# Kernel optimization log

Hardware: AMD Instinct MI355X
Metric: run time of the kernel (lower is better)

Reference implementation:

```python
import jax, jax.numpy as jnp
import numpy as np

B, NA, NB = 2, 2048, 2048
DIM_A, DIM_B = 256, 256
HEADS, DH_A, DH_B = 8, 64, 64
INNER_A, INNER_B = DH_A * HEADS, DH_B * HEADS
EPS = 1e-5


def layer_norm(x, w, b):
    m = jnp.mean(x, axis=-1, keepdims=True)
    v = jnp.mean(jnp.square(x - m), axis=-1, keepdims=True)
    return (x - m) * jax.lax.rsqrt(v + EPS) * w + b


def setup_inputs() -> dict:
    key = jax.random.key(0)
    ks = jax.random.split(key, 16)
    s = 0.02
    return {
        "feat_a": jax.random.normal(ks[0], (B, NA, DIM_A), jnp.float32),
        "feat_b": jax.random.normal(ks[1], (B, NB, DIM_B), jnp.float32),
        "mask_a_b": jax.random.bernoulli(ks[2], 0.5, (B, NA, NB)),
        # linear weights stored (in, out)
        "Wq": jax.random.normal(ks[3], (DIM_A, INNER_B), jnp.float32) * s,
        "bq": jnp.zeros((INNER_B,), jnp.float32),
        "Wk": jax.random.normal(ks[4], (DIM_B, INNER_B), jnp.float32) * s,
        "bk": jnp.zeros((INNER_B,), jnp.float32),
        "Wv": jax.random.normal(ks[5], (DIM_B, INNER_A), jnp.float32) * s,
        "bv": jnp.zeros((INNER_A,), jnp.float32),
        "Wg": jax.random.normal(ks[6], (DIM_A, INNER_A), jnp.float32) * s,
        "bg": jnp.zeros((INNER_A,), jnp.float32),
        "Wo": jax.random.normal(ks[7], (INNER_A, DIM_A), jnp.float32) * s,
        "bo": jnp.zeros((DIM_A,), jnp.float32),
        "ln_a_w": jnp.ones((DIM_A,), jnp.float32),
        "ln_a_b": jnp.zeros((DIM_A,), jnp.float32),
        "ln_b_w": jnp.ones((DIM_B,), jnp.float32),
        "ln_b_b": jnp.zeros((DIM_B,), jnp.float32),
        "qln_w": jnp.ones((INNER_B,), jnp.float32),
        "qln_b": jnp.zeros((INNER_B,), jnp.float32),
        "kln_w": jnp.ones((INNER_B,), jnp.float32),
        "kln_b": jnp.zeros((INNER_B,), jnp.float32),
    }


def reference(feat_a, feat_b, mask_a_b, Wq, bq, Wk, bk, Wv, bv, Wg, bg, Wo, bo,
              ln_a_w, ln_a_b, ln_b_w, ln_b_b, qln_w, qln_b, kln_w, kln_b):
    scale = DH_B ** -0.5
    fa = layer_norm(feat_a, ln_a_w, ln_a_b)            # (b, na, dim_a)
    fb = layer_norm(feat_b, ln_b_w, ln_b_b)            # (b, nb, dim_b)
    q = layer_norm(fa @ Wq + bq, qln_w, qln_b)         # (b, na, inner_b)
    k = layer_norm(fb @ Wk + bk, kln_w, kln_b)         # (b, nb, inner_b)
    v = fb @ Wv + bv                                   # (b, nb, inner_a)
    g = fa @ Wg + bg                                   # (b, na, inner_a)
    q = q.reshape(B, NA, HEADS, DH_B)
    k = k.reshape(B, NB, HEADS, DH_B)
    v = v.reshape(B, NB, HEADS, DH_A)
    g = g.reshape(B, NA, HEADS, DH_A)
    sim = jnp.einsum('bihd,bjhd->bhij', q, k) * scale  # (b, h, na, nb)
    neg = jnp.finfo(sim.dtype).min
    sim = jnp.where(mask_a_b[:, None, :, :], sim, neg)
    attn = jax.nn.softmax(sim, axis=-1)
    out = jnp.einsum('bhij,bjhd->bihd', attn, v)       # (b, na, h, dh_a)
    out = jax.nn.sigmoid(g) * out
    out = out.reshape(B, NA, INNER_A)
    return out @ Wo + bo                               # (b, na, dim_a)
```

## Files before the change

kernel.cpp:

```cpp
#include <hip/hip_runtime.h>
#include <hip/hip_bf16.h>

using bf16 = __hip_bfloat16;
typedef short bf16x8 __attribute__((ext_vector_type(8)));
typedef short bf16x4 __attribute__((ext_vector_type(4)));
typedef float f32x4 __attribute__((ext_vector_type(4)));
typedef unsigned short ushort8_t __attribute__((ext_vector_type(8)));
typedef unsigned long long u64;

static constexpr int NA_ = 2048, NB_ = 2048;
static constexpr int H_ = 8, DH_ = 64, INNER_ = 512;
static constexpr int MROWS = 2 * NA_;

#define MFMA32(a, b, c) __builtin_amdgcn_mfma_f32_16x16x32_bf16(a, b, c, 0, 0, 0)

#if __has_builtin(__builtin_amdgcn_mfma_f32_16x16x16bf16_1k)
#define HAS_MFMA16 1
#define MFMA16(a, b, c) __builtin_amdgcn_mfma_f32_16x16x16bf16_1k(a, b, c, 0, 0, 0)
#elif __has_builtin(__builtin_amdgcn_mfma_f32_16x16x16_bf16)
#define HAS_MFMA16 1
#define MFMA16(a, b, c) __builtin_amdgcn_mfma_f32_16x16x16_bf16(a, b, c, 0, 0, 0)
#else
#define HAS_MFMA16 0
#endif

__device__ __forceinline__ unsigned short bfbits(float x) {
  bf16 h = __float2bfloat16(x);
  return __builtin_bit_cast(unsigned short, h);
}
__device__ __forceinline__ float b2f(unsigned short u) {
  unsigned v = ((unsigned)u) << 16;
  return __builtin_bit_cast(float, v);
}

__global__ __launch_bounds__(256) void ln_feat_kernel(
    const float* __restrict__ fa_in, const float* __restrict__ fb_in,
    const float* __restrict__ law, const float* __restrict__ lab,
    const float* __restrict__ lbw, const float* __restrict__ lbb,
    bf16* __restrict__ fa, bf16* __restrict__ fb) {
  int row = blockIdx.x * 4 + (threadIdx.x >> 6);
  int lane = threadIdx.x & 63;
  const float *src, *w, *bb;
  bf16* dst;
  int r;
  if (row < MROWS) { src = fa_in; w = law; bb = lab; dst = fa; r = row; }
  else             { src = fb_in; w = lbw; bb = lbb; dst = fb; r = row - MROWS; }
  float4 x = *(const float4*)(src + (size_t)r * 256 + lane * 4);
  float s  = (x.x + x.y) + (x.z + x.w);
  float s2 = (x.x * x.x + x.y * x.y) + (x.z * x.z + x.w * x.w);
#pragma unroll
  for (int m = 32; m >= 1; m >>= 1) { s += __shfl_xor(s, m); s2 += __shfl_xor(s2, m); }
  float mean = s * (1.0f / 256.0f);
  float var  = s2 * (1.0f / 256.0f) - mean * mean;
  float rstd = rsqrtf(var + 1e-5f);
  float4 wv = *(const float4*)(w + lane * 4);
  float4 bv = *(const float4*)(bb + lane * 4);
  ushort4 o;
  o.x = bfbits((x.x - mean) * rstd * wv.x + bv.x);
  o.y = bfbits((x.y - mean) * rstd * wv.y + bv.y);
  o.z = bfbits((x.z - mean) * rstd * wv.z + bv.z);
  o.w = bfbits((x.w - mean) * rstd * wv.w + bv.w);
  *(ushort4*)(dst + (size_t)r * 256 + lane * 4) = o;
}

__global__ __launch_bounds__(256) void wconv_kernel(
    const float* __restrict__ Wq, const float* __restrict__ Wk,
    const float* __restrict__ Wv, const float* __restrict__ Wg,
    const float* __restrict__ Wo,
    bf16* __restrict__ Wqt, bf16* __restrict__ Wkt,
    bf16* __restrict__ Wvt, bf16* __restrict__ Wgt,
    bf16* __restrict__ Woth, bf16* __restrict__ Wotl) {
  int z = blockIdx.z;
  int idx = blockIdx.x * 256 + threadIdx.x;
  if (z < 4) {
    const float* W = (z == 0) ? Wq : (z == 1) ? Wk : (z == 2) ? Wv : Wg;
    bf16* Wt = (z == 0) ? Wqt : (z == 1) ? Wkt : (z == 2) ? Wvt : Wgt;
    int kk = idx >> 9, n = idx & 511;
    Wt[n * 256 + kk] = __float2bfloat16(W[idx]);
  } else {
    int kk = idx >> 8, n = idx & 255;
    float w = Wo[idx];
    bf16 hi = __float2bfloat16(w);
    Woth[n * 512 + kk] = hi;
    Wotl[n * 512 + kk] = __float2bfloat16(w - __bfloat162float(hi));
  }
}

__global__ void maskdetect_kernel(const unsigned char* __restrict__ m, int* __restrict__ flag) {
  int t = threadIdx.x;
  if (t == 0) *flag = 0;
  __syncthreads();
  if ((t & 3) != 0 && m[t] != 0) atomicOr(flag, 1);
}

__global__ __launch_bounds__(256) void maskpack_kernel(
    const void* __restrict__ maskp, const int* __restrict__ mflag,
    u64* __restrict__ mbits) {
  const bool m8 = (*mflag != 0);
  int lane = threadIdx.x & 63;
  int wid = threadIdx.x >> 6;
  const size_t NW = 131072;
  for (size_t word = (size_t)blockIdx.x * 4 + wid; word < NW; word += (size_t)gridDim.x * 4) {
    size_t e = word * 64 + lane;
    int v = m8 ? (int)((const unsigned char*)maskp)[e] : ((const int*)maskp)[e];
    u64 bal = __ballot(v != 0);
    if (lane == 0) mbits[word] = bal;
  }
}

__global__ __launch_bounds__(512) void qk_ln_gemm_kernel(
    const bf16* __restrict__ fa, const bf16* __restrict__ fb,
    const bf16* __restrict__ Wqt, const bf16* __restrict__ Wkt,
    const float* __restrict__ bq, const float* __restrict__ bk,
    const float* __restrict__ qlw, const float* __restrict__ qlb,
    const float* __restrict__ klw, const float* __restrict__ klb,
    bf16* __restrict__ qo, bf16* __restrict__ ko) {
  __shared__ __align__(16) bf16 As[32 * 264];
  __shared__ float Pred[32 * 16];
  __shared__ float MV[64];
  int z = blockIdx.y;
  const bf16* A    = z ? fb : fa;
  const bf16* Wt   = z ? Wkt : Wqt;
  const float* bias = z ? bk : bq;
  const float* lw  = z ? klw : qlw;
  const float* lb  = z ? klb : qlb;
  bf16* out        = z ? ko : qo;
  int m0 = blockIdx.x * 32;
  int t = threadIdx.x, wave = t >> 6, lane = t & 63;
  int lm = lane & 15, quad = lane >> 4, q8 = quad * 8;
  int n0w = wave * 64;
#pragma unroll
  for (int i = 0; i < 2; i++) {
    int id = t + 512 * i, r = id >> 5, cg = id & 31;
    *(ushort8_t*)(&As[r * 264 + cg * 8]) =
        *(const ushort8_t*)(A + (size_t)(m0 + r) * 256 + cg * 8);
  }
  __syncthreads();
  f32x4 acc[2][4] = {};
  const bf16* wrow[4];
#pragma unroll
  for (int ni = 0; ni < 4; ni++) wrow[ni] = Wt + (size_t)(n0w + ni * 16 + lm) * 256;
#pragma unroll
  for (int ks = 0; ks < 8; ks++) {
    int k0 = ks * 32;
    bf16x8 bf_[4], af[2];
#pragma unroll
    for (int ni = 0; ni < 4; ni++) bf_[ni] = *(const bf16x8*)(wrow[ni] + k0 + q8);
#pragma unroll
    for (int mi = 0; mi < 2; mi++)
      af[mi] = *(const bf16x8*)(&As[(mi * 16 + lm) * 264 + k0 + q8]);
#pragma unroll
    for (int mi = 0; mi < 2; mi++)
#pragma unroll
      for (int ni = 0; ni < 4; ni++)
        acc[mi][ni] = MFMA32(af[mi], bf_[ni], acc[mi][ni]);
  }
  float bv[4];
#pragma unroll
  for (int ni = 0; ni < 4; ni++) bv[ni] = bias[n0w + ni * 16 + lm];
#pragma unroll
  for (int mi = 0; mi < 2; mi++)
#pragma unroll
    for (int ni = 0; ni < 4; ni++)
#pragma unroll
      for (int r = 0; r < 4; r++) acc[mi][ni][r] += bv[ni];
#pragma unroll
  for (int mi = 0; mi < 2; mi++)
#pragma unroll
    for (int r = 0; r < 4; r++) {
      float s  = (acc[mi][0][r] + acc[mi][1][r]) + (acc[mi][2][r] + acc[mi][3][r]);
      float s2 = (acc[mi][0][r] * acc[mi][0][r] + acc[mi][1][r] * acc[mi][1][r]) +
                 (acc[mi][2][r] * acc[mi][2][r] + acc[mi][3][r] * acc[mi][3][r]);
#pragma unroll
      for (int m = 1; m <= 8; m <<= 1) { s += __shfl_xor(s, m); s2 += __shfl_xor(s2, m); }
      if (lm == 0) {
        int row = mi * 16 + quad * 4 + r;
        Pred[row * 16 + wave * 2]     = s;
        Pred[row * 16 + wave * 2 + 1] = s2;
      }
    }
  __syncthreads();
  if (t < 32) {
    float s = 0.f, s2 = 0.f;
#pragma unroll
    for (int w = 0; w < 8; w++) { s += Pred[t * 16 + w * 2]; s2 += Pred[t * 16 + w * 2 + 1]; }
    float mean = s * (1.0f / 512.0f);
    float var  = s2 * (1.0f / 512.0f) - mean * mean;
    MV[t * 2]     = mean;
    MV[t * 2 + 1] = rsqrtf(var + 1e-5f);
  }
  __syncthreads();
  float lww[4], lbb_[4];
#pragma unroll
  for (int ni = 0; ni < 4; ni++) { lww[ni] = lw[n0w + ni * 16 + lm]; lbb_[ni] = lb[n0w + ni * 16 + lm]; }
#pragma unroll
  for (int mi = 0; mi < 2; mi++)
#pragma unroll
    for (int r = 0; r < 4; r++) {
      int row = mi * 16 + quad * 4 + r;
      float mean = MV[row * 2], rstd = MV[row * 2 + 1];
      size_t obase = (size_t)(m0 + row) * 512 + n0w;
#pragma unroll
      for (int ni = 0; ni < 4; ni++)
        out[obase + ni * 16 + lm] =
            __float2bfloat16((acc[mi][ni][r] - mean) * rstd * lww[ni] + lbb_[ni]);
    }
}

__global__ __launch_bounds__(256) void gv_gemm_kernel(
    const bf16* __restrict__ fa, const bf16* __restrict__ fb,
    const bf16* __restrict__ Wgt, const bf16* __restrict__ Wvt,
    const float* __restrict__ bg, const float* __restrict__ bv,
    bf16* __restrict__ gout, bf16* __restrict__ vout) {
  constexpr int K = 256;
  __shared__ __align__(16) bf16 As[64 * 72];
  __shared__ __align__(16) bf16 Bs[64 * 72];
  int z = blockIdx.z;
  const bf16* A    = z ? fb : fa;
  const bf16* Wt   = z ? Wvt : Wgt;
  const float* bias = z ? bv : bg;
  int n0 = blockIdx.x * 64, m0 = blockIdx.y * 64;
  int t = threadIdx.x, wave = t >> 6, lane = t & 63;
  int lm = lane & 15, quad = lane >> 4, q8 = quad * 8;
  int wm = (wave & 1) * 32, wn = (wave >> 1) * 32;
  f32x4 acc[2][2] = {};
  for (int k0 = 0; k0 < K; k0 += 64) {
    __syncthreads();
#pragma unroll
    for (int i = 0; i < 2; i++) {
      int id = t + 256 * i, r = id >> 3, cg = id & 7;
      *(ushort8_t*)(&As[r * 72 + cg * 8]) =
          *(const ushort8_t*)(A + (size_t)(m0 + r) * K + k0 + cg * 8);
      *(ushort8_t*)(&Bs[r * 72 + cg * 8]) =
          *(const ushort8_t*)(Wt + (size_t)(n0 + r) * K + k0 + cg * 8);
    }
    __syncthreads();
#pragma unroll
    for (int kk = 0; kk < 64; kk += 32) {
      bf16x8 af[2], bf_[2];
#pragma unroll
      for (int i = 0; i < 2; i++) {
        af[i]  = *(const bf16x8*)(&As[(wm + i * 16 + lm) * 72 + kk + q8]);
        bf_[i] = *(const bf16x8*)(&Bs[(wn + i * 16 + lm) * 72 + kk + q8]);
      }
#pragma unroll
      for (int mi = 0; mi < 2; mi++)
#pragma unroll
        for (int ni = 0; ni < 2; ni++)
          acc[mi][ni] = MFMA32(af[mi], bf_[ni], acc[mi][ni]);
    }
  }
  if (z == 0) {
#pragma unroll
    for (int mi = 0; mi < 2; mi++)
#pragma unroll
      for (int ni = 0; ni < 2; ni++) {
        int nn = n0 + wn + ni * 16 + lm;
        float bvv = bias[nn];
        int mb = m0 + wm + mi * 16 + quad * 4;
#pragma unroll
        for (int r = 0; r < 4; r++)
          gout[(size_t)(mb + r) * 512 + nn] = __float2bfloat16(acc[mi][ni][r] + bvv);
      }
  } else {
    __syncthreads();
#pragma unroll
    for (int mi = 0; mi < 2; mi++)
#pragma unroll
      for (int ni = 0; ni < 2; ni++) {
        int d_local = wn + ni * 16 + lm;
        float bvv = bias[n0 + d_local];
        int j_local = wm + mi * 16 + quad * 4;
#pragma unroll
        for (int r = 0; r < 4; r++)
          As[d_local * 72 + j_local + r] = __float2bfloat16(acc[mi][ni][r] + bvv);
      }
    __syncthreads();
    int bidx = m0 >> 11, j0g = m0 & 2047;
    int hh = n0 >> 6;
    int dl = t >> 2, jc = (t & 3) * 16;
    bf16* dstrow = vout + (size_t)((bidx * 8 + hh) * 64 + dl) * 2048 + j0g + jc;
#pragma unroll
    for (int c = 0; c < 4; c++)
      *(ushort4*)(dstrow + c * 4) = *(const ushort4*)(&As[dl * 72 + jc + c * 4]);
  }
}

__global__ __launch_bounds__(256) void attn_kernel(
    const bf16* __restrict__ q, const bf16* __restrict__ k,
    const bf16* __restrict__ vt, const bf16* __restrict__ g,
    const u64* __restrict__ mbits,
    bf16* __restrict__ gh, bf16* __restrict__ gl) {
  __shared__ __align__(16) char smem[45056];
  bf16* Qs = (bf16*)smem;
  bf16* Ks = (bf16*)(smem + 9216);
  bf16* Vs = (bf16*)(smem + 27648);
#if !HAS_MFMA16
  __shared__ __align__(16) bf16 Ps[4][16 * 136];
#endif
  int qt = blockIdx.x, bh = blockIdx.y;
  int bidx = bh >> 3, h = bh & 7;
  int i0 = qt * 64;
  int t = threadIdx.x, wave = t >> 6, lane = t & 63;
  int lm = lane & 15, quad = lane >> 4, q8 = quad * 8;

#pragma unroll
  for (int i = 0; i < 2; i++) {
    int id = t + 256 * i, r = id >> 3, cg = id & 7;
    *(ushort8_t*)(&Qs[r * 72 + cg * 8]) =
        *(const ushort8_t*)(q + (size_t)(bidx * NA_ + i0 + r) * INNER_ + h * DH_ + cg * 8);
  }
  __syncthreads();
  bf16x8 bq0 = *(const bf16x8*)(&Qs[(wave * 16 + lm) * 72 + q8]);
  bf16x8 bq1 = *(const bf16x8*)(&Qs[(wave * 16 + lm) * 72 + 32 + q8]);

  f32x4 oT[4] = {};
  float psum = 0.f;
  const float scale2 = 0.125f * 1.44269504088896f;

  const bf16* kb = k + (size_t)(bidx * NB_) * INNER_ + h * DH_;
  const bf16* vb = vt + (size_t)(bh * DH_) * NB_;
  const u64* mrp = mbits + (size_t)(bidx * NA_ + i0 + wave * 16 + lm) * (NB_ / 64);

  for (int it = 0; it < 16; it++) {
    int j0 = it * 128;
    __syncthreads();
#pragma unroll
    for (int i = 0; i < 4; i++) {
      int id = t + 256 * i;
      {
        int r = id >> 3, cg = id & 7;
        *(ushort8_t*)(&Ks[r * 72 + cg * 8]) =
            *(const ushort8_t*)(kb + (size_t)(j0 + r) * INNER_ + cg * 8);
      }
      {
        int d = id >> 4, jg = id & 15;
        *(ushort8_t*)(&Vs[d * 136 + jg * 8]) =
            *(const ushort8_t*)(vb + (size_t)d * NB_ + j0 + jg * 8);
      }
    }
    u64 w0 = mrp[it * 2] >> (quad * 4);
    u64 w1 = mrp[it * 2 + 1] >> (quad * 4);
    __syncthreads();

    f32x4 st[8];
#pragma unroll
    for (int nt = 0; nt < 8; nt++) {
      bf16x8 a0 = *(const bf16x8*)(&Ks[(nt * 16 + lm) * 72 + q8]);
      bf16x8 a1 = *(const bf16x8*)(&Ks[(nt * 16 + lm) * 72 + 32 + q8]);
      f32x4 a = {0.f, 0.f, 0.f, 0.f};
      a = MFMA32(a0, bq0, a);
      a = MFMA32(a1, bq1, a);
      st[nt] = a;
    }

    bf16x4 pf[8];
#pragma unroll
    for (int nt = 0; nt < 8; nt++) {
      u64 wsel = (nt < 4) ? w0 : w1;
      int base = (nt & 3) * 16;
#pragma unroll
      for (int r = 0; r < 4; r++) {
        float p = exp2f(st[nt][r] * scale2 - 16.0f);
        unsigned live = (unsigned)(wsel >> (base + r)) & 1u;
        st[nt][r] = live ? p : 0.0f;
      }
      psum += (st[nt][0] + st[nt][1]) + (st[nt][2] + st[nt][3]);
      bf16x4 pk;
      pk[0] = (short)bfbits(st[nt][0]);
      pk[1] = (short)bfbits(st[nt][1]);
      pk[2] = (short)bfbits(st[nt][2]);
      pk[3] = (short)bfbits(st[nt][3]);
      pf[nt] = pk;
    }

#if HAS_MFMA16
#pragma unroll
    for (int nt = 0; nt < 8; nt++) {
#pragma unroll
      for (int c = 0; c < 4; c++) {
        bf16x4 vf = *(const bf16x4*)(&Vs[(c * 16 + lm) * 136 + nt * 16 + quad * 4]);
        oT[c] = MFMA16(vf, pf[nt], oT[c]);
      }
    }
#else
#pragma unroll
    for (int nt = 0; nt < 8; nt++)
      *(bf16x4*)(&Ps[wave][lm * 136 + nt * 16 + quad * 4]) = pf[nt];
#pragma unroll
    for (int kb4 = 0; kb4 < 4; kb4++) {
      bf16x8 pfr = *(const bf16x8*)(&Ps[wave][lm * 136 + kb4 * 32 + q8]);
#pragma unroll
      for (int c = 0; c < 4; c++) {
        bf16x8 vf = *(const bf16x8*)(&Vs[(c * 16 + lm) * 136 + kb4 * 32 + q8]);
        oT[c] = MFMA32(vf, pfr, oT[c]);
      }
    }
#endif
  }

  psum += __shfl_xor(psum, 16);
  psum += __shfl_xor(psum, 32);
  float inv = 1.0f / psum;

  size_t gbase = (size_t)(bidx * NA_ + i0 + wave * 16 + lm) * INNER_ + h * DH_;
#pragma unroll
  for (int c = 0; c < 4; c++) {
    int dbase = c * 16 + quad * 4;
    bf16x4 gv4 = *(const bf16x4*)(g + gbase + dbase);
    bf16x4 oh, ol;
#pragma unroll
    for (int r = 0; r < 4; r++) {
      float gvf = b2f((unsigned short)gv4[r]);
      float sig = 1.0f / (1.0f + __expf(-gvf));
      float val = oT[c][r] * inv * sig;
      unsigned short hb = bfbits(val);
      oh[r] = (short)hb;
      ol[r] = (short)bfbits(val - b2f(hb));
    }
    *(bf16x4*)(gh + gbase + dbase) = oh;
    *(bf16x4*)(gl + gbase + dbase) = ol;
  }
}

__global__ __launch_bounds__(256) void gemm_split_kernel(
    const bf16* __restrict__ Ah, const bf16* __restrict__ Al,
    const bf16* __restrict__ Bh, const bf16* __restrict__ Bl,
    const float* __restrict__ bias, float* __restrict__ C) {
  constexpr int K = 512, N = 256;
  __shared__ __align__(16) bf16 Ash[32 * 72];
  __shared__ __align__(16) bf16 Asl[32 * 72];
  __shared__ __align__(16) bf16 Bsh[64 * 72];
  __shared__ __align__(16) bf16 Bsl[64 * 72];
  int n0 = blockIdx.x * 64, m0 = blockIdx.y * 32;
  int t = threadIdx.x, wave = t >> 6, lane = t & 63;
  int lm = lane & 15, quad = lane >> 4, q8 = quad * 8;
  int wm = (wave & 1) * 16, wn = (wave >> 1) * 32;
  f32x4 acc[2] = {};
  for (int k0 = 0; k0 < K; k0 += 64) {
    __syncthreads();
    {
      int r = t >> 3, cg = t & 7;
      size_t ga = (size_t)(m0 + r) * K + k0 + cg * 8;
      *(ushort8_t*)(&Ash[r * 72 + cg * 8]) = *(const ushort8_t*)(Ah + ga);
      *(ushort8_t*)(&Asl[r * 72 + cg * 8]) = *(const ushort8_t*)(Al + ga);
    }
#pragma unroll
    for (int i = 0; i < 2; i++) {
      int id = t + 256 * i, r = id >> 3, cg = id & 7;
      size_t gb = (size_t)(n0 + r) * K + k0 + cg * 8;
      *(ushort8_t*)(&Bsh[r * 72 + cg * 8]) = *(const ushort8_t*)(Bh + gb);
      *(ushort8_t*)(&Bsl[r * 72 + cg * 8]) = *(const ushort8_t*)(Bl + gb);
    }
    __syncthreads();
#pragma unroll
    for (int kk = 0; kk < 64; kk += 32) {
      bf16x8 ah = *(const bf16x8*)(&Ash[(wm + lm) * 72 + kk + q8]);
      bf16x8 al = *(const bf16x8*)(&Asl[(wm + lm) * 72 + kk + q8]);
#pragma unroll
      for (int ni = 0; ni < 2; ni++) {
        bf16x8 bh_ = *(const bf16x8*)(&Bsh[(wn + ni * 16 + lm) * 72 + kk + q8]);
        bf16x8 bl_ = *(const bf16x8*)(&Bsl[(wn + ni * 16 + lm) * 72 + kk + q8]);
        acc[ni] = MFMA32(ah, bh_, acc[ni]);
        acc[ni] = MFMA32(ah, bl_, acc[ni]);
        acc[ni] = MFMA32(al, bh_, acc[ni]);
      }
    }
  }
#pragma unroll
  for (int ni = 0; ni < 2; ni++) {
    int n = n0 + wn + ni * 16 + lm;
    float bvv = bias[n];
    int mb = m0 + wm + quad * 4;
#pragma unroll
    for (int r = 0; r < 4; r++) C[(size_t)(mb + r) * N + n] = acc[ni][r] + bvv;
  }
}

extern "C" void kernel_launch(void* const* d_in, const int* in_sizes, int n_in,
                              void* d_out, int out_size, void* d_ws, size_t ws_size,
                              hipStream_t stream) {
  const float* feat_a = (const float*)d_in[0];
  const float* feat_b = (const float*)d_in[1];
  const void*  mask   = d_in[2];
  const float* Wq = (const float*)d_in[3];
  const float* bq = (const float*)d_in[4];
  const float* Wk = (const float*)d_in[5];
  const float* bk = (const float*)d_in[6];
  const float* Wv = (const float*)d_in[7];
  const float* bv = (const float*)d_in[8];
  const float* Wg = (const float*)d_in[9];
  const float* bg = (const float*)d_in[10];
  const float* Wo = (const float*)d_in[11];
  const float* bo = (const float*)d_in[12];
  const float* law = (const float*)d_in[13];
  const float* lab = (const float*)d_in[14];
  const float* lbw = (const float*)d_in[15];
  const float* lbb = (const float*)d_in[16];
  const float* qlw = (const float*)d_in[17];
  const float* qlb = (const float*)d_in[18];
  const float* klw = (const float*)d_in[19];
  const float* klb = (const float*)d_in[20];

  char* ws = (char*)d_ws;
  size_t off = 0;
  auto alloc = [&](size_t bytes) -> void* {
    void* p = ws + off;
    off += (bytes + 255) & ~(size_t)255;
    return p;
  };
  bf16* fa    = (bf16*)alloc((size_t)MROWS * 256 * 2);
  bf16* fb    = (bf16*)alloc((size_t)MROWS * 256 * 2);
  bf16* Wqt   = (bf16*)alloc((size_t)131072 * 2);
  bf16* Wkt   = (bf16*)alloc((size_t)131072 * 2);
  bf16* Wvt   = (bf16*)alloc((size_t)131072 * 2);
  bf16* Wgt   = (bf16*)alloc((size_t)131072 * 2);
  bf16* Woth  = (bf16*)alloc((size_t)131072 * 2);
  bf16* Wotl  = (bf16*)alloc((size_t)131072 * 2);
  bf16* qb_   = (bf16*)alloc((size_t)MROWS * 512 * 2);
  bf16* kb_   = (bf16*)alloc((size_t)MROWS * 512 * 2);
  bf16* vtb   = (bf16*)alloc((size_t)1024 * 2048 * 2);
  bf16* gbuf  = (bf16*)alloc((size_t)MROWS * 512 * 2);
  bf16* gh    = (bf16*)alloc((size_t)MROWS * 512 * 2);
  bf16* gl    = (bf16*)alloc((size_t)MROWS * 512 * 2);
  u64*  mbits = (u64*)alloc((size_t)131072 * 8);
  int*  mflag = (int*)alloc(256);

  ln_feat_kernel<<<2048, 256, 0, stream>>>(feat_a, feat_b, law, lab, lbw, lbb, fa, fb);
  wconv_kernel<<<dim3(512, 1, 5), 256, 0, stream>>>(Wq, Wk, Wv, Wg, Wo, Wqt, Wkt, Wvt, Wgt, Woth, Wotl);
  maskdetect_kernel<<<1, 256, 0, stream>>>((const unsigned char*)mask, mflag);
  maskpack_kernel<<<2048, 256, 0, stream>>>(mask, mflag, mbits);
  qk_ln_gemm_kernel<<<dim3(128, 2), 512, 0, stream>>>(fa, fb, Wqt, Wkt, bq, bk, qlw, qlb, klw, klb, qb_, kb_);
  gv_gemm_kernel<<<dim3(8, 64, 2), 256, 0, stream>>>(fa, fb, Wgt, Wvt, bg, bv, gbuf, vtb);
  attn_kernel<<<dim3(32, 16), 256, 0, stream>>>(qb_, kb_, vtb, gbuf, mbits, gh, gl);
  gemm_split_kernel<<<dim3(4, 128), 256, 0, stream>>>(gh, gl, Woth, Wotl, bo, (float*)d_out);
}
```

Measured before the change: 234.5 us.

## Merge prep kernels, fuse four projection GEMMs, split attention keys across wave halves

The layernorm, weight conversion, mask detection and mask packing launches are merged into one prep kernel, and the Q/K and G/V projection GEMMs are merged into a single launch with retiled blocks. The attention kernel now runs 512 threads, with two groups of four waves each covering half of the key range. The partial outputs and softmax sums are combined through shared memory, and P goes through LDS into 16x16x32 MFMAs instead of the 16x16x16 path. The aim is fewer launches and more latency hiding in attention, at the cost of extra shared memory, a final reduction step, and scalar stores in the epilogue.

After: 204.0 us. 1.15x faster.

```diff
diff --git a/kernel.cpp b/kernel.cpp
--- a/kernel.cpp
+++ b/kernel.cpp
@@ -3,7 +3,6 @@
 
 using bf16 = __hip_bfloat16;
 typedef short bf16x8 __attribute__((ext_vector_type(8)));
-typedef short bf16x4 __attribute__((ext_vector_type(4)));
 typedef float f32x4 __attribute__((ext_vector_type(4)));
 typedef unsigned short ushort8_t __attribute__((ext_vector_type(8)));
 typedef unsigned long long u64;
@@ -14,16 +13,6 @@
 
 #define MFMA32(a, b, c) __builtin_amdgcn_mfma_f32_16x16x32_bf16(a, b, c, 0, 0, 0)
 
-#if __has_builtin(__builtin_amdgcn_mfma_f32_16x16x16bf16_1k)
-#define HAS_MFMA16 1
-#define MFMA16(a, b, c) __builtin_amdgcn_mfma_f32_16x16x16bf16_1k(a, b, c, 0, 0, 0)
-#elif __has_builtin(__builtin_amdgcn_mfma_f32_16x16x16_bf16)
-#define HAS_MFMA16 1
-#define MFMA16(a, b, c) __builtin_amdgcn_mfma_f32_16x16x16_bf16(a, b, c, 0, 0, 0)
-#else
-#define HAS_MFMA16 0
-#endif
-
 __device__ __forceinline__ unsigned short bfbits(float x) {
   bf16 h = __float2bfloat16(x);
   return __builtin_bit_cast(unsigned short, h);
@@ -33,319 +22,309 @@
   return __builtin_bit_cast(float, v);
 }
 
-__global__ __launch_bounds__(256) void ln_feat_kernel(
+__global__ __launch_bounds__(256) void prep_kernel(
     const float* __restrict__ fa_in, const float* __restrict__ fb_in,
     const float* __restrict__ law, const float* __restrict__ lab,
     const float* __restrict__ lbw, const float* __restrict__ lbb,
-    bf16* __restrict__ fa, bf16* __restrict__ fb) {
-  int row = blockIdx.x * 4 + (threadIdx.x >> 6);
-  int lane = threadIdx.x & 63;
-  const float *src, *w, *bb;
-  bf16* dst;
-  int r;
-  if (row < MROWS) { src = fa_in; w = law; bb = lab; dst = fa; r = row; }
-  else             { src = fb_in; w = lbw; bb = lbb; dst = fb; r = row - MROWS; }
-  float4 x = *(const float4*)(src + (size_t)r * 256 + lane * 4);
-  float s  = (x.x + x.y) + (x.z + x.w);
-  float s2 = (x.x * x.x + x.y * x.y) + (x.z * x.z + x.w * x.w);
-#pragma unroll
-  for (int m = 32; m >= 1; m >>= 1) { s += __shfl_xor(s, m); s2 += __shfl_xor(s2, m); }
-  float mean = s * (1.0f / 256.0f);
-  float var  = s2 * (1.0f / 256.0f) - mean * mean;
-  float rstd = rsqrtf(var + 1e-5f);
-  float4 wv = *(const float4*)(w + lane * 4);
-  float4 bv = *(const float4*)(bb + lane * 4);
-  ushort4 o;
-  o.x = bfbits((x.x - mean) * rstd * wv.x + bv.x);
-  o.y = bfbits((x.y - mean) * rstd * wv.y + bv.y);
-  o.z = bfbits((x.z - mean) * rstd * wv.z + bv.z);
-  o.w = bfbits((x.w - mean) * rstd * wv.w + bv.w);
-  *(ushort4*)(dst + (size_t)r * 256 + lane * 4) = o;
-}
-
-__global__ __launch_bounds__(256) void wconv_kernel(
+    bf16* __restrict__ fa, bf16* __restrict__ fb,
     const float* __restrict__ Wq, const float* __restrict__ Wk,
     const float* __restrict__ Wv, const float* __restrict__ Wg,
     const float* __restrict__ Wo,
     bf16* __restrict__ Wqt, bf16* __restrict__ Wkt,
     bf16* __restrict__ Wvt, bf16* __restrict__ Wgt,
-    bf16* __restrict__ Woth, bf16* __restrict__ Wotl) {
-  int z = blockIdx.z;
-  int idx = blockIdx.x * 256 + threadIdx.x;
-  if (z < 4) {
-    const float* W = (z == 0) ? Wq : (z == 1) ? Wk : (z == 2) ? Wv : Wg;
-    bf16* Wt = (z == 0) ? Wqt : (z == 1) ? Wkt : (z == 2) ? Wvt : Wgt;
-    int kk = idx >> 9, n = idx & 511;
-    Wt[n * 256 + kk] = __float2bfloat16(W[idx]);
+    bf16* __restrict__ Woth, bf16* __restrict__ Wotl,
+    const void* __restrict__ maskp, u64* __restrict__ mbits) {
+  int blk = blockIdx.x;
+  int t = threadIdx.x;
+  if (blk < 2048) {
+    int row = blk * 4 + (t >> 6);
+    int lane = t & 63;
+    const float *src, *w, *bb;
+    bf16* dst;
+    int r;
+    if (row < MROWS) { src = fa_in; w = law; bb = lab; dst = fa; r = row; }
+    else             { src = fb_in; w = lbw; bb = lbb; dst = fb; r = row - MROWS; }
+    float4 x = *(const float4*)(src + (size_t)r * 256 + lane * 4);
+    float s  = (x.x + x.y) + (x.z + x.w);
+    float s2 = (x.x * x.x + x.y * x.y) + (x.z * x.z + x.w * x.w);
+#pragma unroll
+    for (int m = 32; m >= 1; m >>= 1) { s += __shfl_xor(s, m); s2 += __shfl_xor(s2, m); }
+    float mean = s * (1.0f / 256.0f);
+    float var  = s2 * (1.0f / 256.0f) - mean * mean;
+    float rstd = rsqrtf(var + 1e-5f);
+    float4 wv = *(const float4*)(w + lane * 4);
+    float4 bv = *(const float4*)(bb + lane * 4);
+    ushort4 o;
+    o.x = bfbits((x.x - mean) * rstd * wv.x + bv.x);
+    o.y = bfbits((x.y - mean) * rstd * wv.y + bv.y);
+    o.z = bfbits((x.z - mean) * rstd * wv.z + bv.z);
+    o.w = bfbits((x.w - mean) * rstd * wv.w + bv.w);
+    *(ushort4*)(dst + (size_t)r * 256 + lane * 4) = o;
+  } else if (blk < 4608) {
+    int z = (blk - 2048) >> 9;
+    int idx = ((blk - 2048) & 511) * 256 + t;
+    if (z < 4) {
+      const float* W = (z == 0) ? Wq : (z == 1) ? Wk : (z == 2) ? Wv : Wg;
+      bf16* Wt = (z == 0) ? Wqt : (z == 1) ? Wkt : (z == 2) ? Wvt : Wgt;
+      int kk = idx >> 9, n = idx & 511;
+      Wt[n * 256 + kk] = __float2bfloat16(W[idx]);
+    } else {
+      int kk = idx >> 8, n = idx & 255;
+      float w = Wo[idx];
+      bf16 hi = __float2bfloat16(w);
+      Woth[n * 512 + kk] = hi;
+      Wotl[n * 512 + kk] = __float2bfloat16(w - __bfloat162float(hi));
+    }
   } else {
-    int kk = idx >> 8, n = idx & 255;
-    float w = Wo[idx];
-    bf16 hi = __float2bfloat16(w);
-    Woth[n * 512 + kk] = hi;
-    Wotl[n * 512 + kk] = __float2bfloat16(w - __bfloat162float(hi));
-  }
-}
-
-__global__ void maskdetect_kernel(const unsigned char* __restrict__ m, int* __restrict__ flag) {
-  int t = threadIdx.x;
-  if (t == 0) *flag = 0;
-  __syncthreads();
-  if ((t & 3) != 0 && m[t] != 0) atomicOr(flag, 1);
-}
-
-__global__ __launch_bounds__(256) void maskpack_kernel(
-    const void* __restrict__ maskp, const int* __restrict__ mflag,
-    u64* __restrict__ mbits) {
-  const bool m8 = (*mflag != 0);
-  int lane = threadIdx.x & 63;
-  int wid = threadIdx.x >> 6;
-  const size_t NW = 131072;
-  for (size_t word = (size_t)blockIdx.x * 4 + wid; word < NW; word += (size_t)gridDim.x * 4) {
-    size_t e = word * 64 + lane;
-    int v = m8 ? (int)((const unsigned char*)maskp)[e] : ((const int*)maskp)[e];
-    u64 bal = __ballot(v != 0);
-    if (lane == 0) mbits[word] = bal;
-  }
-}
-
-__global__ __launch_bounds__(512) void qk_ln_gemm_kernel(
+    __shared__ unsigned shf[4];
+    const unsigned char* mu = (const unsigned char*)maskp;
+    bool nz = ((t & 3) != 0) && (mu[t] != 0);
+    u64 bal = __ballot(nz);
+    if ((t & 63) == 0) shf[t >> 6] = (bal != 0ull) ? 1u : 0u;
+    __syncthreads();
+    bool m8 = (shf[0] | shf[1] | shf[2] | shf[3]) != 0;
+    int lane = t & 63, wid = t >> 6;
+    int lb = blk - 4608;
+    for (size_t word = (size_t)lb * 4 + wid; word < 131072; word += 8192) {
+      size_t e = word * 64 + lane;
+      int v = m8 ? (int)mu[e] : ((const int*)maskp)[e];
+      u64 b2 = __ballot(v != 0);
+      if (lane == 0) mbits[word] = b2;
+    }
+  }
+}
+
+__global__ __launch_bounds__(256) void gemm4_kernel(
     const bf16* __restrict__ fa, const bf16* __restrict__ fb,
     const bf16* __restrict__ Wqt, const bf16* __restrict__ Wkt,
+    const bf16* __restrict__ Wgt, const bf16* __restrict__ Wvt,
     const float* __restrict__ bq, const float* __restrict__ bk,
+    const float* __restrict__ bg, const float* __restrict__ bv,
     const float* __restrict__ qlw, const float* __restrict__ qlb,
     const float* __restrict__ klw, const float* __restrict__ klb,
-    bf16* __restrict__ qo, bf16* __restrict__ ko) {
-  __shared__ __align__(16) bf16 As[32 * 264];
-  __shared__ float Pred[32 * 16];
-  __shared__ float MV[64];
-  int z = blockIdx.y;
-  const bf16* A    = z ? fb : fa;
-  const bf16* Wt   = z ? Wkt : Wqt;
-  const float* bias = z ? bk : bq;
-  const float* lw  = z ? klw : qlw;
-  const float* lb  = z ? klb : qlb;
-  bf16* out        = z ? ko : qo;
-  int m0 = blockIdx.x * 32;
+    bf16* __restrict__ qo, bf16* __restrict__ ko,
+    bf16* __restrict__ gout, bf16* __restrict__ vout) {
+  __shared__ __align__(16) char sm[27648];
+  int z = blockIdx.z;
   int t = threadIdx.x, wave = t >> 6, lane = t & 63;
   int lm = lane & 15, quad = lane >> 4, q8 = quad * 8;
-  int n0w = wave * 64;
-#pragma unroll
-  for (int i = 0; i < 2; i++) {
-    int id = t + 512 * i, r = id >> 5, cg = id & 31;
-    *(ushort8_t*)(&As[r * 264 + cg * 8]) =
-        *(const ushort8_t*)(A + (size_t)(m0 + r) * 256 + cg * 8);
-  }
-  __syncthreads();
-  f32x4 acc[2][4] = {};
-  const bf16* wrow[4];
-#pragma unroll
-  for (int ni = 0; ni < 4; ni++) wrow[ni] = Wt + (size_t)(n0w + ni * 16 + lm) * 256;
-#pragma unroll
-  for (int ks = 0; ks < 8; ks++) {
-    int k0 = ks * 32;
-    bf16x8 bf_[4], af[2];
-#pragma unroll
-    for (int ni = 0; ni < 4; ni++) bf_[ni] = *(const bf16x8*)(wrow[ni] + k0 + q8);
-#pragma unroll
-    for (int mi = 0; mi < 2; mi++)
-      af[mi] = *(const bf16x8*)(&As[(mi * 16 + lm) * 264 + k0 + q8]);
-#pragma unroll
-    for (int mi = 0; mi < 2; mi++)
-#pragma unroll
-      for (int ni = 0; ni < 4; ni++)
-        acc[mi][ni] = MFMA32(af[mi], bf_[ni], acc[mi][ni]);
-  }
-  float bv[4];
-#pragma unroll
-  for (int ni = 0; ni < 4; ni++) bv[ni] = bias[n0w + ni * 16 + lm];
-#pragma unroll
-  for (int mi = 0; mi < 2; mi++)
-#pragma unroll
-    for (int ni = 0; ni < 4; ni++)
-#pragma unroll
-      for (int r = 0; r < 4; r++) acc[mi][ni][r] += bv[ni];
-#pragma unroll
-  for (int mi = 0; mi < 2; mi++)
+
+  if (z < 2) {
+    bf16* As = (bf16*)sm;
+    float* Pred = (float*)(sm + 16896);
+    float* MV   = (float*)(sm + 17408);
+    const bf16* A    = z ? fb : fa;
+    const bf16* Wt   = z ? Wkt : Wqt;
+    const float* bias = z ? bk : bq;
+    const float* lw  = z ? klw : qlw;
+    const float* lb  = z ? klb : qlb;
+    bf16* out        = z ? ko : qo;
+    int m0 = blockIdx.x * 16;
+#pragma unroll
+    for (int i = 0; i < 2; i++) {
+      int id = t + 256 * i, r = id >> 5, cg = id & 31;
+      *(ushort8_t*)(&As[r * 264 + cg * 8]) =
+          *(const ushort8_t*)(A + (size_t)(m0 + r) * 256 + cg * 8);
+    }
+    __syncthreads();
+    int n0w = wave * 128;
+    f32x4 acc[8] = {};
+    const bf16* wrow[8];
+#pragma unroll
+    for (int ni = 0; ni < 8; ni++) wrow[ni] = Wt + (size_t)(n0w + ni * 16 + lm) * 256;
+#pragma unroll
+    for (int ks = 0; ks < 8; ks++) {
+      int k0 = ks * 32;
+      bf16x8 af = *(const bf16x8*)(&As[lm * 264 + k0 + q8]);
+#pragma unroll
+      for (int ni = 0; ni < 8; ni++) {
+        bf16x8 bf_ = *(const bf16x8*)(wrow[ni] + k0 + q8);
+        acc[ni] = MFMA32(af, bf_, acc[ni]);
+      }
+    }
+    float bvv[8];
+#pragma unroll
+    for (int ni = 0; ni < 8; ni++) bvv[ni] = bias[n0w + ni * 16 + lm];
+#pragma unroll
+    for (int ni = 0; ni < 8; ni++)
+#pragma unroll
+      for (int r = 0; r < 4; r++) acc[ni][r] += bvv[ni];
 #pragma unroll
     for (int r = 0; r < 4; r++) {
-      float s  = (acc[mi][0][r] + acc[mi][1][r]) + (acc[mi][2][r] + acc[mi][3][r]);
-      float s2 = (acc[mi][0][r] * acc[mi][0][r] + acc[mi][1][r] * acc[mi][1][r]) +
-                 (acc[mi][2][r] * acc[mi][2][r] + acc[mi][3][r] * acc[mi][3][r]);
+      float s = 0.f, s2 = 0.f;
+#pragma unroll
+      for (int ni = 0; ni < 8; ni++) { s += acc[ni][r]; s2 += acc[ni][r] * acc[ni][r]; }
 #pragma unroll
       for (int m = 1; m <= 8; m <<= 1) { s += __shfl_xor(s, m); s2 += __shfl_xor(s2, m); }
       if (lm == 0) {
-        int row = mi * 16 + quad * 4 + r;
-        Pred[row * 16 + wave * 2]     = s;
-        Pred[row * 16 + wave * 2 + 1] = s2;
-      }
-    }
-  __syncthreads();
-  if (t < 32) {
-    float s = 0.f, s2 = 0.f;
-#pragma unroll
-    for (int w = 0; w < 8; w++) { s += Pred[t * 16 + w * 2]; s2 += Pred[t * 16 + w * 2 + 1]; }
-    float mean = s * (1.0f / 512.0f);
-    float var  = s2 * (1.0f / 512.0f) - mean * mean;
-    MV[t * 2]     = mean;
-    MV[t * 2 + 1] = rsqrtf(var + 1e-5f);
-  }
-  __syncthreads();
-  float lww[4], lbb_[4];
-#pragma unroll
-  for (int ni = 0; ni < 4; ni++) { lww[ni] = lw[n0w + ni * 16 + lm]; lbb_[ni] = lb[n0w + ni * 16 + lm]; }
-#pragma unroll
-  for (int mi = 0; mi < 2; mi++)
+        int row = quad * 4 + r;
+        Pred[row * 8 + wave * 2]     = s;
+        Pred[row * 8 + wave * 2 + 1] = s2;
+      }
+    }
+    __syncthreads();
+    if (t < 16) {
+      float s = 0.f, s2 = 0.f;
+#pragma unroll
+      for (int w = 0; w < 4; w++) { s += Pred[t * 8 + w * 2]; s2 += Pred[t * 8 + w * 2 + 1]; }
+      float mean = s * (1.0f / 512.0f);
+      float var  = s2 * (1.0f / 512.0f) - mean * mean;
+      MV[t * 2]     = mean;
+      MV[t * 2 + 1] = rsqrtf(var + 1e-5f);
+    }
+    __syncthreads();
+    float lww[8], lbb_[8];
+#pragma unroll
+    for (int ni = 0; ni < 8; ni++) {
+      lww[ni]  = lw[n0w + ni * 16 + lm];
+      lbb_[ni] = lb[n0w + ni * 16 + lm];
+    }
 #pragma unroll
     for (int r = 0; r < 4; r++) {
-      int row = mi * 16 + quad * 4 + r;
+      int row = quad * 4 + r;
       float mean = MV[row * 2], rstd = MV[row * 2 + 1];
       size_t obase = (size_t)(m0 + row) * 512 + n0w;
 #pragma unroll
-      for (int ni = 0; ni < 4; ni++)
+      for (int ni = 0; ni < 8; ni++)
         out[obase + ni * 16 + lm] =
-            __float2bfloat16((acc[mi][ni][r] - mean) * rstd * lww[ni] + lbb_[ni]);
-    }
-}
-
-__global__ __launch_bounds__(256) void gv_gemm_kernel(
-    const bf16* __restrict__ fa, const bf16* __restrict__ fb,
-    const bf16* __restrict__ Wgt, const bf16* __restrict__ Wvt,
-    const float* __restrict__ bg, const float* __restrict__ bv,
-    bf16* __restrict__ gout, bf16* __restrict__ vout) {
-  constexpr int K = 256;
-  __shared__ __align__(16) bf16 As[64 * 72];
-  __shared__ __align__(16) bf16 Bs[64 * 72];
-  int z = blockIdx.z;
-  const bf16* A    = z ? fb : fa;
-  const bf16* Wt   = z ? Wvt : Wgt;
-  const float* bias = z ? bv : bg;
-  int n0 = blockIdx.x * 64, m0 = blockIdx.y * 64;
-  int t = threadIdx.x, wave = t >> 6, lane = t & 63;
-  int lm = lane & 15, quad = lane >> 4, q8 = quad * 8;
-  int wm = (wave & 1) * 32, wn = (wave >> 1) * 32;
-  f32x4 acc[2][2] = {};
-  for (int k0 = 0; k0 < K; k0 += 64) {
-    __syncthreads();
-#pragma unroll
-    for (int i = 0; i < 2; i++) {
-      int id = t + 256 * i, r = id >> 3, cg = id & 7;
-      *(ushort8_t*)(&As[r * 72 + cg * 8]) =
-          *(const ushort8_t*)(A + (size_t)(m0 + r) * K + k0 + cg * 8);
-      *(ushort8_t*)(&Bs[r * 72 + cg * 8]) =
-          *(const ushort8_t*)(Wt + (size_t)(n0 + r) * K + k0 + cg * 8);
-    }
-    __syncthreads();
-#pragma unroll
-    for (int kk = 0; kk < 64; kk += 32) {
-      bf16x8 af[2], bf_[2];
+            __float2bfloat16((acc[ni][r] - mean) * rstd * lww[ni] + lbb_[ni]);
+    }
+  } else {
+    bf16* As = (bf16*)sm;
+    bf16* Bs = (bf16*)(sm + 18432);
+    const bf16* A    = (z == 3) ? fb : fa;
+    const bf16* Wt   = (z == 3) ? Wvt : Wgt;
+    const float* bias = (z == 3) ? bv : bg;
+    int x = blockIdx.x;
+    int m0 = (x >> 3) * 128, n0 = (x & 7) * 64;
+    int wm = wave * 32;
+    f32x4 acc[2][4] = {};
+    for (int k0 = 0; k0 < 256; k0 += 64) {
+      __syncthreads();
+#pragma unroll
+      for (int i = 0; i < 4; i++) {
+        int id = t + 256 * i, r = id >> 3, cg = id & 7;
+        *(ushort8_t*)(&As[r * 72 + cg * 8]) =
+            *(const ushort8_t*)(A + (size_t)(m0 + r) * 256 + k0 + cg * 8);
+      }
 #pragma unroll
       for (int i = 0; i < 2; i++) {
-        af[i]  = *(const bf16x8*)(&As[(wm + i * 16 + lm) * 72 + kk + q8]);
-        bf_[i] = *(const bf16x8*)(&Bs[(wn + i * 16 + lm) * 72 + kk + q8]);
-      }
+        int id = t + 256 * i, r = id >> 3, cg = id & 7;
+        *(ushort8_t*)(&Bs[r * 72 + cg * 8]) =
+            *(const ushort8_t*)(Wt + (size_t)(n0 + r) * 256 + k0 + cg * 8);
+      }
+      __syncthreads();
+#pragma unroll
+      for (int kk = 0; kk < 64; kk += 32) {
+        bf16x8 af[2], bf_[4];
+#pragma unroll
+        for (int mi = 0; mi < 2; mi++)
+          af[mi] = *(const bf16x8*)(&As[(wm + mi * 16 + lm) * 72 + kk + q8]);
+#pragma unroll
+        for (int ni = 0; ni < 4; ni++)
+          bf_[ni] = *(const bf16x8*)(&Bs[(ni * 16 + lm) * 72 + kk + q8]);
+#pragma unroll
+        for (int mi = 0; mi < 2; mi++)
+#pragma unroll
+          for (int ni = 0; ni < 4; ni++)
+            acc[mi][ni] = MFMA32(af[mi], bf_[ni], acc[mi][ni]);
+      }
+    }
+    if (z == 2) {
 #pragma unroll
       for (int mi = 0; mi < 2; mi++)
 #pragma unroll
-        for (int ni = 0; ni < 2; ni++)
-          acc[mi][ni] = MFMA32(af[mi], bf_[ni], acc[mi][ni]);
-    }
-  }
-  if (z == 0) {
-#pragma unroll
-    for (int mi = 0; mi < 2; mi++)
-#pragma unroll
-      for (int ni = 0; ni < 2; ni++) {
-        int nn = n0 + wn + ni * 16 + lm;
-        float bvv = bias[nn];
-        int mb = m0 + wm + mi * 16 + quad * 4;
-#pragma unroll
-        for (int r = 0; r < 4; r++)
-          gout[(size_t)(mb + r) * 512 + nn] = __float2bfloat16(acc[mi][ni][r] + bvv);
-      }
-  } else {
-    __syncthreads();
-#pragma unroll
-    for (int mi = 0; mi < 2; mi++)
-#pragma unroll
-      for (int ni = 0; ni < 2; ni++) {
-        int d_local = wn + ni * 16 + lm;
-        float bvv = bias[n0 + d_local];
-        int j_local = wm + mi * 16 + quad * 4;
-#pragma unroll
-        for (int r = 0; r < 4; r++)
-          As[d_local * 72 + j_local + r] = __float2bfloat16(acc[mi][ni][r] + bvv);
-      }
-    __syncthreads();
-    int bidx = m0 >> 11, j0g = m0 & 2047;
-    int hh = n0 >> 6;
-    int dl = t >> 2, jc = (t & 3) * 16;
-    bf16* dstrow = vout + (size_t)((bidx * 8 + hh) * 64 + dl) * 2048 + j0g + jc;
-#pragma unroll
-    for (int c = 0; c < 4; c++)
-      *(ushort4*)(dstrow + c * 4) = *(const ushort4*)(&As[dl * 72 + jc + c * 4]);
-  }
-}
-
-__global__ __launch_bounds__(256) void attn_kernel(
+        for (int ni = 0; ni < 4; ni++) {
+          int nn = n0 + ni * 16 + lm;
+          float bvv = bias[nn];
+          int mb = m0 + wm + mi * 16 + quad * 4;
+#pragma unroll
+          for (int r = 0; r < 4; r++)
+            gout[(size_t)(mb + r) * 512 + nn] = __float2bfloat16(acc[mi][ni][r] + bvv);
+        }
+    } else {
+      __syncthreads();
+      bf16* buf = (bf16*)sm;
+#pragma unroll
+      for (int mi = 0; mi < 2; mi++)
+#pragma unroll
+        for (int ni = 0; ni < 4; ni++) {
+          int d_local = ni * 16 + lm;
+          float bvv = bias[n0 + d_local];
+          int j_local = wm + mi * 16 + quad * 4;
+#pragma unroll
+          for (int r = 0; r < 4; r++)
+            buf[d_local * 136 + j_local + r] = __float2bfloat16(acc[mi][ni][r] + bvv);
+        }
+      __syncthreads();
+      int bidx2 = m0 >> 11, j0g = m0 & 2047, hh = n0 >> 6;
+      int dl = t >> 2, jseg = (t & 3) * 32;
+      bf16* dstrow = vout + (size_t)((bidx2 * 8 + hh) * 64 + dl) * 2048 + j0g + jseg;
+#pragma unroll
+      for (int c = 0; c < 4; c++)
+        *(ushort8_t*)(dstrow + c * 8) = *(const ushort8_t*)(&buf[dl * 136 + jseg + c * 8]);
+    }
+  }
+}
+
+__global__ __launch_bounds__(512) void attn_kernel(
     const bf16* __restrict__ q, const bf16* __restrict__ k,
     const bf16* __restrict__ vt, const bf16* __restrict__ g,
     const u64* __restrict__ mbits,
     bf16* __restrict__ gh, bf16* __restrict__ gl) {
-  __shared__ __align__(16) char smem[45056];
+  __shared__ __align__(16) char smem[65024];
   bf16* Qs = (bf16*)smem;
-  bf16* Ks = (bf16*)(smem + 9216);
-  bf16* Vs = (bf16*)(smem + 27648);
-#if !HAS_MFMA16
-  __shared__ __align__(16) bf16 Ps[4][16 * 136];
-#endif
+  bf16* KsB = (bf16*)(smem + 9216);
+  bf16* VsB = (bf16*)(smem + 27648);
+  bf16* PsB = (bf16*)(smem + 46080);
+  float* Om = (float*)(smem + 9216);
+  float* Lbuf = (float*)(smem + 64512);
+
   int qt = blockIdx.x, bh = blockIdx.y;
   int bidx = bh >> 3, h = bh & 7;
   int i0 = qt * 64;
   int t = threadIdx.x, wave = t >> 6, lane = t & 63;
+  int jhalf = wave >> 2, w4 = wave & 3;
   int lm = lane & 15, quad = lane >> 4, q8 = quad * 8;
-
-#pragma unroll
-  for (int i = 0; i < 2; i++) {
-    int id = t + 256 * i, r = id >> 3, cg = id & 7;
+  int lt = t & 255;
+
+  {
+    int r = t >> 3, cg = t & 7;
     *(ushort8_t*)(&Qs[r * 72 + cg * 8]) =
         *(const ushort8_t*)(q + (size_t)(bidx * NA_ + i0 + r) * INNER_ + h * DH_ + cg * 8);
   }
   __syncthreads();
-  bf16x8 bq0 = *(const bf16x8*)(&Qs[(wave * 16 + lm) * 72 + q8]);
-  bf16x8 bq1 = *(const bf16x8*)(&Qs[(wave * 16 + lm) * 72 + 32 + q8]);
-
-  f32x4 oT[4] = {};
+  bf16x8 bq0 = *(const bf16x8*)(&Qs[(w4 * 16 + lm) * 72 + q8]);
+  bf16x8 bq1 = *(const bf16x8*)(&Qs[(w4 * 16 + lm) * 72 + 32 + q8]);
+
+  f32x4 oacc[4] = {};
   float psum = 0.f;
   const float scale2 = 0.125f * 1.44269504088896f;
 
   const bf16* kb = k + (size_t)(bidx * NB_) * INNER_ + h * DH_;
   const bf16* vb = vt + (size_t)(bh * DH_) * NB_;
-  const u64* mrp = mbits + (size_t)(bidx * NA_ + i0 + wave * 16 + lm) * (NB_ / 64);
+  bf16* Pw = PsB + wave * (16 * 72);
+  bf16* Ks = KsB + jhalf * (64 * 72);
+  bf16* Vs = VsB + jhalf * (64 * 72);
+  const u64* mrp = mbits + ((size_t)(bidx * NA_ + i0 + w4 * 16 + lm)) * (NB_ / 64) + jhalf * 16;
 
   for (int it = 0; it < 16; it++) {
-    int j0 = it * 128;
-    __syncthreads();
-#pragma unroll
-    for (int i = 0; i < 4; i++) {
-      int id = t + 256 * i;
-      {
-        int r = id >> 3, cg = id & 7;
-        *(ushort8_t*)(&Ks[r * 72 + cg * 8]) =
-            *(const ushort8_t*)(kb + (size_t)(j0 + r) * INNER_ + cg * 8);
-      }
-      {
-        int d = id >> 4, jg = id & 15;
-        *(ushort8_t*)(&Vs[d * 136 + jg * 8]) =
-            *(const ushort8_t*)(vb + (size_t)d * NB_ + j0 + jg * 8);
-      }
-    }
-    u64 w0 = mrp[it * 2] >> (quad * 4);
-    u64 w1 = mrp[it * 2 + 1] >> (quad * 4);
-    __syncthreads();
-
-    f32x4 st[8];
-#pragma unroll
-    for (int nt = 0; nt < 8; nt++) {
+    int j0 = jhalf * 1024 + it * 64;
+    __syncthreads();
+#pragma unroll
+    for (int i = 0; i < 2; i++) {
+      int id = lt + 256 * i, r = id >> 3, cg = id & 7;
+      *(ushort8_t*)(&Ks[r * 72 + cg * 8]) =
+          *(const ushort8_t*)(kb + (size_t)(j0 + r) * INNER_ + cg * 8);
+      *(ushort8_t*)(&Vs[r * 72 + cg * 8]) =
+          *(const ushort8_t*)(vb + (size_t)r * NB_ + j0 + cg * 8);
+    }
+    u64 sm = mrp[it] >> (quad * 4);
+    __syncthreads();
+
+    f32x4 st[4];
+#pragma unroll
+    for (int nt = 0; nt < 4; nt++) {
       bf16x8 a0 = *(const bf16x8*)(&Ks[(nt * 16 + lm) * 72 + q8]);
       bf16x8 a1 = *(const bf16x8*)(&Ks[(nt * 16 + lm) * 72 + 32 + q8]);
       f32x4 a = {0.f, 0.f, 0.f, 0.f};
@@ -354,72 +333,79 @@
       st[nt] = a;
     }
 
-    bf16x4 pf[8];
-#pragma unroll
-    for (int nt = 0; nt < 8; nt++) {
-      u64 wsel = (nt < 4) ? w0 : w1;
-      int base = (nt & 3) * 16;
+    float pr[4][4];
+#pragma unroll
+    for (int nt = 0; nt < 4; nt++)
 #pragma unroll
       for (int r = 0; r < 4; r++) {
         float p = exp2f(st[nt][r] * scale2 - 16.0f);
-        unsigned live = (unsigned)(wsel >> (base + r)) & 1u;
-        st[nt][r] = live ? p : 0.0f;
-      }
-      psum += (st[nt][0] + st[nt][1]) + (st[nt][2] + st[nt][3]);
-      bf16x4 pk;
-      pk[0] = (short)bfbits(st[nt][0]);
-      pk[1] = (short)bfbits(st[nt][1]);
-      pk[2] = (short)bfbits(st[nt][2]);
-      pk[3] = (short)bfbits(st[nt][3]);
-      pf[nt] = pk;
-    }
-
-#if HAS_MFMA16
-#pragma unroll
-    for (int nt = 0; nt < 8; nt++) {
-#pragma unroll
-      for (int c = 0; c < 4; c++) {
-        bf16x4 vf = *(const bf16x4*)(&Vs[(c * 16 + lm) * 136 + nt * 16 + quad * 4]);
-        oT[c] = MFMA16(vf, pf[nt], oT[c]);
-      }
-    }
-#else
-#pragma unroll
-    for (int nt = 0; nt < 8; nt++)
-      *(bf16x4*)(&Ps[wave][lm * 136 + nt * 16 + quad * 4]) = pf[nt];
-#pragma unroll
-    for (int kb4 = 0; kb4 < 4; kb4++) {
-      bf16x8 pfr = *(const bf16x8*)(&Ps[wave][lm * 136 + kb4 * 32 + q8]);
-#pragma unroll
-      for (int c = 0; c < 4; c++) {
-        bf16x8 vf = *(const bf16x8*)(&Vs[(c * 16 + lm) * 136 + kb4 * 32 + q8]);
-        oT[c] = MFMA32(vf, pfr, oT[c]);
-      }
-    }
-#endif
+        unsigned live = (unsigned)(sm >> (nt * 16 + r)) & 1u;
+        pr[nt][r] = live ? p : 0.0f;
+      }
+
+    float s0 = (pr[0][0] + pr[0][1]) + (pr[0][2] + pr[0][3]);
+    float s1 = (pr[1][0] + pr[1][1]) + (pr[1][2] + pr[1][3]);
+    float s2 = (pr[2][0] + pr[2][1]) + (pr[2][2] + pr[2][3]);
+    float s3 = (pr[3][0] + pr[3][1]) + (pr[3][2] + pr[3][3]);
+    psum += (s0 + s1) + (s2 + s3);
+
+#pragma unroll
+    for (int nt = 0; nt < 4; nt++) {
+      ushort4 pk;
+      pk.x = bfbits(pr[nt][0]);
+      pk.y = bfbits(pr[nt][1]);
+      pk.z = bfbits(pr[nt][2]);
+      pk.w = bfbits(pr[nt][3]);
+      *(ushort4*)(Pw + lm * 72 + nt * 16 + quad * 4) = pk;
+    }
+
+    bf16x8 ap0 = *(const bf16x8*)(&Pw[lm * 72 + q8]);
+    bf16x8 ap1 = *(const bf16x8*)(&Pw[lm * 72 + 32 + q8]);
+#pragma unroll
+    for (int c = 0; c < 4; c++) {
+      bf16x8 v0 = *(const bf16x8*)(&Vs[(c * 16 + lm) * 72 + q8]);
+      bf16x8 v1 = *(const bf16x8*)(&Vs[(c * 16 + lm) * 72 + 32 + q8]);
+      oacc[c] = MFMA32(ap0, v0, oacc[c]);
+      oacc[c] = MFMA32(ap1, v1, oacc[c]);
+    }
   }
 
   psum += __shfl_xor(psum, 16);
   psum += __shfl_xor(psum, 32);
-  float inv = 1.0f / psum;
-
-  size_t gbase = (size_t)(bidx * NA_ + i0 + wave * 16 + lm) * INNER_ + h * DH_;
-#pragma unroll
-  for (int c = 0; c < 4; c++) {
-    int dbase = c * 16 + quad * 4;
-    bf16x4 gv4 = *(const bf16x4*)(g + gbase + dbase);
-    bf16x4 oh, ol;
+
+  __syncthreads();
+  if (quad == 0) Lbuf[jhalf * 64 + w4 * 16 + lm] = psum;
+  if (jhalf == 1) {
+#pragma unroll
+    for (int c = 0; c < 4; c++)
+#pragma unroll
+      for (int r = 0; r < 4; r++)
+        Om[w4 * (16 * 66) + (quad * 4 + r) * 66 + c * 16 + lm] = oacc[c][r];
+  }
+  __syncthreads();
+  if (jhalf == 0) {
+    int mrow = i0 + w4 * 16 + quad * 4;
+    float inv[4];
 #pragma unroll
     for (int r = 0; r < 4; r++) {
-      float gvf = b2f((unsigned short)gv4[r]);
-      float sig = 1.0f / (1.0f + __expf(-gvf));
-      float val = oT[c][r] * inv * sig;
-      unsigned short hb = bfbits(val);
-      oh[r] = (short)hb;
-      ol[r] = (short)bfbits(val - b2f(hb));
-    }
-    *(bf16x4*)(gh + gbase + dbase) = oh;
-    *(bf16x4*)(gl + gbase + dbase) = ol;
+      float l = Lbuf[w4 * 16 + quad * 4 + r] + Lbuf[64 + w4 * 16 + quad * 4 + r];
+      inv[r] = 1.0f / l;
+    }
+#pragma unroll
+    for (int c = 0; c < 4; c++) {
+      int col = h * DH_ + c * 16 + lm;
+#pragma unroll
+      for (int r = 0; r < 4; r++) {
+        float o = oacc[c][r] + Om[w4 * (16 * 66) + (quad * 4 + r) * 66 + c * 16 + lm];
+        size_t idx = (size_t)(bidx * NA_ + mrow + r) * INNER_ + col;
+        float gv = b2f(__builtin_bit_cast(unsigned short, g[idx]));
+        float sig = 1.0f / (1.0f + __expf(-gv));
+        float val = o * inv[r] * sig;
+        unsigned short hb = bfbits(val);
+        gh[idx] = __builtin_bit_cast(bf16, hb);
+        gl[idx] = __float2bfloat16(val - b2f(hb));
+      }
+    }
   }
 }
 
@@ -524,14 +510,13 @@
   bf16* gh    = (bf16*)alloc((size_t)MROWS * 512 * 2);
   bf16* gl    = (bf16*)alloc((size_t)MROWS * 512 * 2);
   u64*  mbits = (u64*)alloc((size_t)131072 * 8);
-  int*  mflag = (int*)alloc(256);
-
-  ln_feat_kernel<<<2048, 256, 0, stream>>>(feat_a, feat_b, law, lab, lbw, lbb, fa, fb);
-  wconv_kernel<<<dim3(512, 1, 5), 256, 0, stream>>>(Wq, Wk, Wv, Wg, Wo, Wqt, Wkt, Wvt, Wgt, Woth, Wotl);
-  maskdetect_kernel<<<1, 256, 0, stream>>>((const unsigned char*)mask, mflag);
-  maskpack_kernel<<<2048, 256, 0, stream>>>(mask, mflag, mbits);
-  qk_ln_gemm_kernel<<<dim3(128, 2), 512, 0, stream>>>(fa, fb, Wqt, Wkt, bq, bk, qlw, qlb, klw, klb, qb_, kb_);
-  gv_gemm_kernel<<<dim3(8, 64, 2), 256, 0, stream>>>(fa, fb, Wgt, Wvt, bg, bv, gbuf, vtb);
-  attn_kernel<<<dim3(32, 16), 256, 0, stream>>>(qb_, kb_, vtb, gbuf, mbits, gh, gl);
+
+  prep_kernel<<<6656, 256, 0, stream>>>(
+      feat_a, feat_b, law, lab, lbw, lbb, fa, fb,
+      Wq, Wk, Wv, Wg, Wo, Wqt, Wkt, Wvt, Wgt, Woth, Wotl, mask, mbits);
+  gemm4_kernel<<<dim3(256, 1, 4), 256, 0, stream>>>(
+      fa, fb, Wqt, Wkt, Wgt, Wvt, bq, bk, bg, bv,
+      qlw, qlb, klw, klb, qb_, kb_, gbuf, vtb);
+  attn_kernel<<<dim3(32, 16), 512, 0, stream>>>(qb_, kb_, vtb, gbuf, mbits, gh, gl);
   gemm_split_kernel<<<dim3(4, 128), 256, 0, stream>>>(gh, gl, Woth, Wotl, bo, (float*)d_out);
 }
```
